# Kernel tuning notes

Hardware: AMD Instinct MI355X
Metric: run time of the kernel (lower is better)

The kernel has to match this reference:

```python
import jax, jax.numpy as jnp
import numpy as np

B, T = 8, 1024
D = 256          # n_embd
NH = 4           # n_head
MULT = 4         # mlp_internal_dim_multiplier
GRID = 32        # grid_size, T == GRID*GRID
NLAYER = 3
N = D * MULT // NH   # sparse head dim = 256
EPS = 1e-5


def _freqs_2d(h, w, dim, theta=10000.0):
    # matches get_freqs_2d_fixed: returns (h*w, dim//2) complex64
    dim_half = dim // 2
    freqs = 1.0 / theta ** (np.arange(0, dim_half, 2, dtype=np.float32) / dim_half)
    fx = np.outer(np.arange(w, dtype=np.float32), freqs)
    fy = np.outer(np.arange(h, dtype=np.float32), freqs)
    cx = np.exp(1j * fx).astype(np.complex64)          # (w, dim_half/2)
    cy = np.exp(1j * fy).astype(np.complex64)          # (h, dim_half/2)
    gx = np.broadcast_to(cx[None, :, :], (h, w, cx.shape[-1]))
    gy = np.broadcast_to(cy[:, None, :], (h, w, cy.shape[-1]))
    return np.concatenate([gx, gy], axis=-1).reshape(h * w, -1)

FREQS = jnp.asarray(_freqs_2d(GRID, GRID, N))  # (T, N//2) complex64


def _rope(x):
    # x: (B, nh, T, N) real -> complex pairs, rotate, back to real
    xc = x.reshape(*x.shape[:-1], -1, 2)
    xc = jax.lax.complex(xc[..., 0], xc[..., 1])       # (B, nh, T, N/2)
    xr = xc * FREQS[None, None, :, :]
    out = jnp.stack([jnp.real(xr), jnp.imag(xr)], axis=-1)
    return out.reshape(x.shape).astype(x.dtype)


def _ln(x):
    # LayerNorm over last dim, no affine (biased variance, like torch)
    m = jnp.mean(x, axis=-1, keepdims=True)
    v = jnp.var(x, axis=-1, keepdims=True)
    return (x - m) / jnp.sqrt(v + EPS)


def setup_inputs() -> dict:
    key = jax.random.key(0)
    ks = jax.random.split(key, 6)
    std = 0.02
    return {
        "inputs": jax.random.normal(ks[0], (B, T), dtype=jnp.float32),
        "in_w": jax.random.normal(ks[1], (D, 1), dtype=jnp.float32) * std,
        "in_b": jnp.zeros((D,), dtype=jnp.float32),
        "encoder": jax.random.normal(ks[2], (NH, D, N), dtype=jnp.float32) * std,
        "encoder_v": jax.random.normal(ks[3], (NH, D, N), dtype=jnp.float32) * std,
        "decoder": jax.random.normal(ks[4], (NH * N, D), dtype=jnp.float32) * std,
        "out_w": jax.random.normal(ks[5], (1, D), dtype=jnp.float32) * std,
        "out_b": jnp.zeros((1,), dtype=jnp.float32),
    }


def reference(inputs, in_w, in_b, encoder, encoder_v, decoder, out_w, out_b):
    # input projection: (B,T,1) @ (1,D) + b -> (B,T,D)
    x = inputs[..., None] * in_w[None, None, :, 0].swapaxes(-1, -1)  # placeholder
    x = inputs[..., None] @ in_w.T + in_b                            # (B,T,D)
    x = _ln(x)
    scale = 1.0 / jnp.sqrt(jnp.asarray(N, dtype=x.dtype))
    for _ in range(NLAYER):
        # encoder: (B,T,D) x (nh,D,N) -> (B,nh,T,N)
        x_sparse = jax.nn.relu(jnp.einsum('btd,hdn->bhtn', x, encoder))
        QR = _rope(x_sparse)
        KR = _rope(x_sparse)
        scores = jnp.einsum('bhtn,bhsn->bhts', QR, KR) * scale       # (B,nh,T,T)
        attn = jax.nn.softmax(scores, axis=-1)
        yKV = jnp.einsum('bhts,bsd->bhtd', attn, x)                  # V = x, broadcast over heads
        yKV = _ln(yKV)
        y_sparse = jax.nn.relu(jnp.einsum('bhtd,hdn->bhtn', yKV, encoder_v))
        xy_sparse = x_sparse * y_sparse                              # (B,nh,T,N)
        # (B,nh,T,N) -> (B,T,nh*N) @ (nh*N,D) -> (B,T,D)
        yMLP = xy_sparse.transpose(0, 2, 1, 3).reshape(B, T, NH * N) @ decoder
        x = _ln(x + _ln(yMLP))
    logits = x @ out_w.T + out_b                                     # (B,T,1)
    return logits
```

## Files before the change

kernel.cpp:

```cpp
#include <hip/hip_runtime.h>
#include <hip/hip_bf16.h>
#include <math.h>

#define B_ 8
#define T_ 1024
#define D_ 256
#define NH_ 4
#define N_ 256
#define EPS_ 1e-5f

typedef __attribute__((ext_vector_type(8))) short short8_t;
typedef __attribute__((ext_vector_type(4))) float floatx4;

__device__ inline unsigned short f2bf(float f) {
    unsigned u = __builtin_bit_cast(unsigned, f);
    u += 0x7FFFu + ((u >> 16) & 1u);
    return (unsigned short)(u >> 16);
}
__device__ inline float bf2f(unsigned short h) {
    return __builtin_bit_cast(float, (unsigned)h << 16);
}

__device__ inline void gload_lds16(const unsigned short* g, unsigned short* l) {
    __builtin_amdgcn_global_load_lds(
        (const __attribute__((address_space(1))) unsigned int*)g,
        (__attribute__((address_space(3))) unsigned int*)l, 16, 0, 0);
}

__device__ inline float2 block_stats_256(float v, float* red) {
    float s1 = v, s2 = v * v;
    #pragma unroll
    for (int o = 32; o > 0; o >>= 1) { s1 += __shfl_down(s1, o); s2 += __shfl_down(s2, o); }
    int wave = threadIdx.x >> 6, lane = threadIdx.x & 63;
    __syncthreads();
    if (lane == 0) { red[wave] = s1; red[4 + wave] = s2; }
    __syncthreads();
    float S1 = red[0] + red[1] + red[2] + red[3];
    float S2 = red[4] + red[5] + red[6] + red[7];
    float mean = S1 * (1.f / 256.f);
    float var  = S2 * (1.f / 256.f) - mean * mean;
    return make_float2(mean, var);
}

__global__ __launch_bounds__(256) void k_wT(
    const float* __restrict__ in, unsigned short* __restrict__ outh,
    unsigned short* __restrict__ outl, int R, int C)
{
    __shared__ float tile[64][65];
    int c0 = blockIdx.x * 64, r0 = blockIdx.y * 64, h = blockIdx.z;
    in += (size_t)h * R * C;
    for (int i = threadIdx.x; i < 4096; i += 256) {
        int r = i >> 6, c = i & 63;
        tile[r][c] = in[(size_t)(r0 + r) * C + c0 + c];
    }
    __syncthreads();
    for (int i = threadIdx.x; i < 4096; i += 256) {
        int c = i >> 6, r = i & 63;
        float v = tile[r][c];
        unsigned short hb = f2bf(v);
        size_t o = (size_t)(h * C + c0 + c) * R + r0 + r;
        outh[o] = hb;
        outl[o] = f2bf(v - bf2f(hb));
    }
}

__global__ __launch_bounds__(256) void k_input_ln(
    const float* __restrict__ inputs, const float* __restrict__ in_w,
    const float* __restrict__ in_b, float* __restrict__ x,
    unsigned short* __restrict__ xh, unsigned short* __restrict__ xl)
{
    __shared__ float red[8];
    int row = blockIdx.x;
    int d = threadIdx.x;
    float v = inputs[row] * in_w[d] + in_b[d];
    float2 mv = block_stats_256(v, red);
    float o = (v - mv.x) * rsqrtf(mv.y + EPS_);
    size_t idx = (size_t)row * D_ + d;
    x[idx] = o;
    unsigned short hb = f2bf(o);
    xh[idx] = hb;
    xl[idx] = f2bf(o - bf2f(hb));
}

#define PG 40
template<int MODE>
__global__ __launch_bounds__(256, 2) void k_gemm_mfma(
    const unsigned short* __restrict__ Ah, const unsigned short* __restrict__ Al,
    const unsigned short* __restrict__ Wh, const unsigned short* __restrict__ Wl,
    const unsigned short* __restrict__ xsh, const unsigned short* __restrict__ xsl,
    unsigned short* __restrict__ outh, unsigned short* __restrict__ outl,
    float* __restrict__ outf)
{
    constexpr int K = (MODE == 2) ? 1024 : 256;
    __shared__ unsigned short As_h[128 * PG], As_l[128 * PG];
    __shared__ unsigned short Ws_h[128 * PG], Ws_l[128 * PG];
    int tid = threadIdx.x;
    int w = tid >> 6, lane = tid & 63, quad = lane >> 4, l16 = lane & 15;
    int wm = w >> 1, wn = w & 1;
    int m0 = blockIdx.y * 128, n0x = blockIdx.x * 128;
    size_t a_row0, w_row0, out_row0;
    int col0;
    int koff = 0, kend = K;
    if (MODE == 1) {
        int bh = blockIdx.z;
        a_row0 = (size_t)bh * 1024 + m0;
        w_row0 = (size_t)((bh & 3) * 256 + n0x);
        out_row0 = (size_t)(bh >> 2) * 1024 + m0;
        col0 = (bh & 3) * 256 + n0x;
    } else {
        a_row0 = m0; w_row0 = n0x; out_row0 = m0; col0 = n0x;
        if (MODE == 2) { koff = blockIdx.z * 256; kend = koff + 256; }
    }
    floatx4 acc[4][4];
    #pragma unroll
    for (int mt = 0; mt < 4; mt++)
        #pragma unroll
        for (int nt = 0; nt < 4; nt++)
            acc[mt][nt] = (floatx4){0.f, 0.f, 0.f, 0.f};

    for (int k0 = koff; k0 < kend; k0 += 32) {
        #pragma unroll
        for (int it = 0; it < 2; it++) {
            int fl = tid + it * 256;
            int row = fl >> 2, ch = fl & 3;
            size_t ga = (a_row0 + row) * (size_t)K + k0 + ch * 8;
            size_t gw = (w_row0 + row) * (size_t)K + k0 + ch * 8;
            *(short8_t*)&As_h[row * PG + ch * 8] = *(const short8_t*)(Ah + ga);
            *(short8_t*)&As_l[row * PG + ch * 8] = *(const short8_t*)(Al + ga);
            *(short8_t*)&Ws_h[row * PG + ch * 8] = *(const short8_t*)(Wh + gw);
            *(short8_t*)&Ws_l[row * PG + ch * 8] = *(const short8_t*)(Wl + gw);
        }
        __syncthreads();
        short8_t afh[4], afl[4], bfh[4], bfl[4];
        #pragma unroll
        for (int mt = 0; mt < 4; mt++) {
            afh[mt] = *(const short8_t*)&As_h[(wm * 64 + mt * 16 + l16) * PG + quad * 8];
            afl[mt] = *(const short8_t*)&As_l[(wm * 64 + mt * 16 + l16) * PG + quad * 8];
        }
        #pragma unroll
        for (int nt = 0; nt < 4; nt++) {
            bfh[nt] = *(const short8_t*)&Ws_h[(wn * 64 + nt * 16 + l16) * PG + quad * 8];
            bfl[nt] = *(const short8_t*)&Ws_l[(wn * 64 + nt * 16 + l16) * PG + quad * 8];
        }
        #pragma unroll
        for (int mt = 0; mt < 4; mt++)
            #pragma unroll
            for (int nt = 0; nt < 4; nt++) {
                acc[mt][nt] = __builtin_amdgcn_mfma_f32_16x16x32_bf16(afh[mt], bfh[nt], acc[mt][nt], 0, 0, 0);
                acc[mt][nt] = __builtin_amdgcn_mfma_f32_16x16x32_bf16(afh[mt], bfl[nt], acc[mt][nt], 0, 0, 0);
                acc[mt][nt] = __builtin_amdgcn_mfma_f32_16x16x32_bf16(afl[mt], bfh[nt], acc[mt][nt], 0, 0, 0);
            }
        __syncthreads();
    }

    #pragma unroll
    for (int mt = 0; mt < 4; mt++) {
        #pragma unroll
        for (int r = 0; r < 4; r++) {
            size_t grow = out_row0 + wm * 64 + mt * 16 + quad * 4 + r;
            #pragma unroll
            for (int nt = 0; nt < 4; nt++) {
                int gcol = col0 + wn * 64 + nt * 16 + l16;
                float v = acc[mt][nt][r];
                if (MODE == 0) {
                    v = fmaxf(v, 0.f);
                    size_t o = grow * 1024 + gcol;
                    unsigned short hb = f2bf(v);
                    outh[o] = hb;
                    outl[o] = f2bf(v - bf2f(hb));
                } else if (MODE == 1) {
                    float y = fmaxf(v, 0.f);
                    size_t o = grow * 1024 + gcol;
                    float xv = bf2f(xsh[o]) + bf2f(xsl[o]);
                    float p = xv * y;
                    unsigned short hb = f2bf(p);
                    outh[o] = hb;
                    outl[o] = f2bf(p - bf2f(hb));
                } else {
                    outf[(size_t)blockIdx.z * 2097152 + grow * 256 + gcol] = v;
                }
            }
        }
    }
}

__global__ __launch_bounds__(256) void k_rope_bf16(
    const unsigned short* __restrict__ xsh, const unsigned short* __restrict__ xsl,
    unsigned short* __restrict__ qh, unsigned short* __restrict__ ql)
{
    int tid = blockIdx.x * 256 + threadIdx.x;
    int e0 = tid * 8;
    int n0 = e0 & 255;
    int t  = (e0 >> 8) & 1023;
    int bh = e0 >> 18;
    int h = bh & 3, b = bh >> 2;
    size_t src = (((size_t)(b * T_ + t) * NH_ + h) << 8) + n0;
    short8_t vh = *(const short8_t*)(xsh + src);
    short8_t vl = *(const short8_t*)(xsl + src);
    float v[8];
    #pragma unroll
    for (int i = 0; i < 8; i++)
        v[i] = bf2f((unsigned short)vh[i]) + bf2f((unsigned short)vl[i]);
    float cc[4], ss[4];
    int p0 = n0 >> 1;
    #pragma unroll
    for (int i = 0; i < 4; i++) {
        int p = p0 + i;
        int j = p & 63;
        int pos = (p < 64) ? (t & 31) : (t >> 5);
        float f = powf(10000.f, -(float)j * (1.f / 64.f));
        float ang = (float)pos * f;
        sincosf(ang, &ss[i], &cc[i]);
    }
    float r[8];
    r[0] = v[0] * cc[0] - v[1] * ss[0];
    r[1] = v[0] * ss[0] + v[1] * cc[0];
    r[2] = v[2] * cc[1] - v[3] * ss[1];
    r[3] = v[2] * ss[1] + v[3] * cc[1];
    r[4] = v[4] * cc[2] - v[5] * ss[2];
    r[5] = v[4] * ss[2] + v[5] * cc[2];
    r[6] = v[6] * cc[3] - v[7] * ss[3];
    r[7] = v[6] * ss[3] + v[7] * cc[3];
    short8_t oh, ol;
    #pragma unroll
    for (int i = 0; i < 8; i++) {
        unsigned short hbits = f2bf(r[i]);
        oh[i] = (short)hbits;
        ol[i] = (short)f2bf(r[i] - bf2f(hbits));
    }
    *(short8_t*)(qh + e0) = oh;
    *(short8_t*)(ql + e0) = ol;
}

__global__ __launch_bounds__(256) void k_xT(const float* __restrict__ x,
                                            unsigned short* __restrict__ Vfh,
                                            unsigned short* __restrict__ Vfl)
{
    __shared__ float tile[64][65];
    int t0 = blockIdx.x * 64, d0 = blockIdx.y * 64, b = blockIdx.z;
    const float* src = x + ((size_t)b * T_ + t0) * D_ + d0;
    for (int i = threadIdx.x; i < 1024; i += 256) {
        int r = i >> 4, c = i & 15;
        float4 v = *(const float4*)(src + (size_t)r * D_ + c * 4);
        tile[r][c * 4 + 0] = v.x;
        tile[r][c * 4 + 1] = v.y;
        tile[r][c * 4 + 2] = v.z;
        tile[r][c * 4 + 3] = v.w;
    }
    __syncthreads();
    for (int i = threadIdx.x; i < 1024; i += 256) {
        int d = i >> 4, c = i & 15;
        int tg = t0 + c * 4;
        int jj = tg >> 5, qd = (tg >> 3) & 3, i8 = tg & 7;
        int dg = d0 + d;
        int tn = dg >> 4, s16 = dg & 15;
        size_t o = (((size_t)b * 32 + jj) * 16 + tn) * 512 + (qd * 16 + s16) * 8 + i8;
        float v0 = tile[c * 4 + 0][d], v1 = tile[c * 4 + 1][d];
        float v2 = tile[c * 4 + 2][d], v3 = tile[c * 4 + 3][d];
        ushort4 oh, ol;
        oh.x = f2bf(v0); ol.x = f2bf(v0 - bf2f(oh.x));
        oh.y = f2bf(v1); ol.y = f2bf(v1 - bf2f(oh.y));
        oh.z = f2bf(v2); ol.z = f2bf(v2 - bf2f(oh.z));
        oh.w = f2bf(v3); ol.w = f2bf(v3 - bf2f(oh.w));
        *(ushort4*)(Vfh + o) = oh;
        *(ushort4*)(Vfl + o) = ol;
    }
}

#define PPW 36

__global__ __launch_bounds__(512, 1) void k_attn_mfma(
    const unsigned short* __restrict__ qr_h, const unsigned short* __restrict__ qr_l,
    const unsigned short* __restrict__ Vf_h, const unsigned short* __restrict__ Vf_l,
    unsigned short* __restrict__ ykvh, unsigned short* __restrict__ ykvl)
{
    __shared__ unsigned short K_h[2][16 * 512];
    __shared__ unsigned short K_l[2][16 * 512];
    __shared__ unsigned short V_h[2][16 * 512];
    __shared__ unsigned short V_l[2][16 * 512];
    __shared__ unsigned short P_h[8][16 * PPW];
    __shared__ unsigned short P_l[8][16 * PPW];

    int tid = threadIdx.x;
    int w = tid >> 6, lane = tid & 63, quad = lane >> 4, l16 = lane & 15;
    int gid = blockIdx.x;
    int bh = gid & 31, tile = gid >> 5, b = bh >> 2;
    int t0q = tile * 128;
    const unsigned short* qhb = qr_h + (size_t)bh * T_ * N_;
    const unsigned short* qlb = qr_l + (size_t)bh * T_ * N_;
    const unsigned short* vhb = Vf_h + (size_t)b * 32 * 16 * 512;
    const unsigned short* vlb = Vf_l + (size_t)b * 32 * 16 * 512;

    short8_t qfh[8], qfl[8];
    #pragma unroll
    for (int kc = 0; kc < 8; kc++) {
        size_t o = (size_t)(t0q + w * 16 + l16) * N_ + kc * 32 + quad * 8;
        qfh[kc] = *(const short8_t*)(qhb + o);
        qfl[kc] = *(const short8_t*)(qlb + o);
    }

    floatx4 O[16];
    #pragma unroll
    for (int tn = 0; tn < 16; tn++) O[tn] = (floatx4){0.f, 0.f, 0.f, 0.f};
    float lst[4] = {0.f, 0.f, 0.f, 0.f};
    const float scale = 0.0625f;

    #pragma unroll
    for (int s = 0; s < 2; s++) {
        int slot = w * 2 + s;
        int ct = slot >> 3, kc = slot & 7;
        size_t go = (size_t)(ct * 16 + l16) * N_ + kc * 32 + quad * 8;
        gload_lds16(qhb + go, &K_h[0][slot * 512]);
        gload_lds16(qlb + go, &K_l[0][slot * 512]);
        size_t vo = ((size_t)slot << 9) + lane * 8;
        gload_lds16(vhb + vo, &V_h[0][slot * 512]);
        gload_lds16(vlb + vo, &V_l[0][slot * 512]);
    }

    for (int j = 0; j < 32; j++) {
        int buf = j & 1;
        __syncthreads();
        if (j < 31) {
            #pragma unroll
            for (int s = 0; s < 2; s++) {
                int slot = w * 2 + s;
                int ct = slot >> 3, kc = slot & 7;
                size_t go = (size_t)((j + 1) * 32 + ct * 16 + l16) * N_ + kc * 32 + quad * 8;
                gload_lds16(qhb + go, &K_h[buf ^ 1][slot * 512]);
                gload_lds16(qlb + go, &K_l[buf ^ 1][slot * 512]);
                size_t vo = ((size_t)((j + 1) * 16 + slot) << 9) + lane * 8;
                gload_lds16(vhb + vo, &V_h[buf ^ 1][slot * 512]);
                gload_lds16(vlb + vo, &V_l[buf ^ 1][slot * 512]);
            }
        }

        floatx4 sc[2];
        #pragma unroll
        for (int ct = 0; ct < 2; ct++) {
            floatx4 a_hh = (floatx4){0.f, 0.f, 0.f, 0.f};
            floatx4 a_hl = (floatx4){0.f, 0.f, 0.f, 0.f};
            floatx4 a_lh = (floatx4){0.f, 0.f, 0.f, 0.f};
            #pragma unroll
            for (int kc = 0; kc < 8; kc++) {
                short8_t bkh = *(const short8_t*)&K_h[buf][(ct * 8 + kc) * 512 + lane * 8];
                short8_t bkl = *(const short8_t*)&K_l[buf][(ct * 8 + kc) * 512 + lane * 8];
                a_hh = __builtin_amdgcn_mfma_f32_16x16x32_bf16(qfh[kc], bkh, a_hh, 0, 0, 0);
                a_hl = __builtin_amdgcn_mfma_f32_16x16x32_bf16(qfh[kc], bkl, a_hl, 0, 0, 0);
                a_lh = __builtin_amdgcn_mfma_f32_16x16x32_bf16(qfl[kc], bkh, a_lh, 0, 0, 0);
            }
            sc[ct] = (a_hh + a_hl) + a_lh;
        }

        #pragma unroll
        for (int r = 0; r < 4; r++) {
            float p0 = __expf(sc[0][r] * scale - 8.f);
            float p1 = __expf(sc[1][r] * scale - 8.f);
            lst[r] += p0 + p1;
            unsigned short p0h = f2bf(p0), p1h = f2bf(p1);
            P_h[w][(quad * 4 + r) * PPW + l16]      = p0h;
            P_h[w][(quad * 4 + r) * PPW + 16 + l16] = p1h;
            P_l[w][(quad * 4 + r) * PPW + l16]      = f2bf(p0 - bf2f(p0h));
            P_l[w][(quad * 4 + r) * PPW + 16 + l16] = f2bf(p1 - bf2f(p1h));
        }

        short8_t pah = *(const short8_t*)&P_h[w][l16 * PPW + quad * 8];
        short8_t pal = *(const short8_t*)&P_l[w][l16 * PPW + quad * 8];

        #pragma unroll
        for (int tn = 0; tn < 16; tn++) {
            short8_t vbh = *(const short8_t*)&V_h[buf][tn * 512 + lane * 8];
            short8_t vbl = *(const short8_t*)&V_l[buf][tn * 512 + lane * 8];
            O[tn] = __builtin_amdgcn_mfma_f32_16x16x32_bf16(pah, vbh, O[tn], 0, 0, 0);
            O[tn] = __builtin_amdgcn_mfma_f32_16x16x32_bf16(pah, vbl, O[tn], 0, 0, 0);
            O[tn] = __builtin_amdgcn_mfma_f32_16x16x32_bf16(pal, vbh, O[tn], 0, 0, 0);
        }
    }

    size_t obase = ((size_t)bh * T_ + t0q + w * 16) * D_;
    #pragma unroll
    for (int r = 0; r < 4; r++) {
        float lsum = lst[r];
        #pragma unroll
        for (int o = 1; o < 16; o <<= 1) lsum += __shfl_xor(lsum, o);
        float li = 1.f / lsum;
        float s1 = 0.f, s2 = 0.f;
        #pragma unroll
        for (int tn = 0; tn < 16; tn++) { float v = O[tn][r]; s1 += v; s2 += v * v; }
        #pragma unroll
        for (int o = 1; o < 16; o <<= 1) { s1 += __shfl_xor(s1, o); s2 += __shfl_xor(s2, o); }
        float mean = s1 * li * (1.f / 256.f);
        float e2   = s2 * li * li * (1.f / 256.f);
        float var  = e2 - mean * mean;
        float rs = rsqrtf(var + EPS_);
        float a = li * rs, bb = mean * rs;
        int row = quad * 4 + r;
        #pragma unroll
        for (int tn = 0; tn < 16; tn++) {
            float v = O[tn][r] * a - bb;
            size_t o = obase + (size_t)row * D_ + tn * 16 + l16;
            unsigned short hb = f2bf(v);
            ykvh[o] = hb;
            ykvl[o] = f2bf(v - bf2f(hb));
        }
    }
}

__global__ __launch_bounds__(256) void k_resid_ln(float* __restrict__ x,
                                                  const float* __restrict__ ymlp,
                                                  unsigned short* __restrict__ xh,
                                                  unsigned short* __restrict__ xl)
{
    __shared__ float red[8];
    int row = blockIdx.x, d = threadIdx.x;
    size_t o = (size_t)row * D_ + d;
    float y = ymlp[o] + ymlp[o + 2097152] + ymlp[o + 2 * 2097152] + ymlp[o + 3 * 2097152];
    float2 mv1 = block_stats_256(y, red);
    float v = x[o] + (y - mv1.x) * rsqrtf(mv1.y + EPS_);
    float2 mv2 = block_stats_256(v, red);
    float out = (v - mv2.x) * rsqrtf(mv2.y + EPS_);
    x[o] = out;
    unsigned short hb = f2bf(out);
    xh[o] = hb;
    xl[o] = f2bf(out - bf2f(hb));
}

__global__ __launch_bounds__(256) void k_logits(
    const float* __restrict__ x, const float* __restrict__ out_w,
    const float* __restrict__ out_b, float* __restrict__ out)
{
    __shared__ float red[4];
    int row = blockIdx.x, d = threadIdx.x;
    float v = x[(size_t)row * D_ + d] * out_w[d];
    #pragma unroll
    for (int o = 32; o > 0; o >>= 1) v += __shfl_down(v, o);
    int wave = d >> 6, lane = d & 63;
    if (lane == 0) red[wave] = v;
    __syncthreads();
    if (d == 0) out[row] = red[0] + red[1] + red[2] + red[3] + out_b[0];
}

extern "C" void kernel_launch(void* const* d_in, const int* in_sizes, int n_in,
                              void* d_out, int out_size, void* d_ws, size_t ws_size,
                              hipStream_t stream)
{
    (void)in_sizes; (void)n_in; (void)out_size;
    if (ws_size < ((size_t)115 << 20)) return;

    const float* inputs    = (const float*)d_in[0];
    const float* in_w      = (const float*)d_in[1];
    const float* in_b      = (const float*)d_in[2];
    const float* encoder   = (const float*)d_in[3];
    const float* encoder_v = (const float*)d_in[4];
    const float* decoder   = (const float*)d_in[5];
    const float* out_w     = (const float*)d_in[6];
    const float* out_b     = (const float*)d_in[7];

    char* wsb = (char*)d_ws;
    float* x             = (float*)(wsb);
    unsigned short* x_h  = (unsigned short*)(wsb + ((size_t)8  << 20));
    unsigned short* x_l  = (unsigned short*)(wsb + ((size_t)12 << 20));
    unsigned short* Vf_h = x_h;
    unsigned short* Vf_l = x_l;
    unsigned short* xs_h = (unsigned short*)(wsb + ((size_t)16 << 20));
    unsigned short* xs_l = (unsigned short*)(wsb + ((size_t)32 << 20));
    float* ymlp          = (float*)(wsb + ((size_t)16 << 20));
    unsigned short* qr_h = (unsigned short*)(wsb + ((size_t)48 << 20));
    unsigned short* qr_l = (unsigned short*)(wsb + ((size_t)64 << 20));
    unsigned short* xy_h = qr_h;
    unsigned short* xy_l = qr_l;
    unsigned short* ykv_h = (unsigned short*)(wsb + ((size_t)80 << 20));
    unsigned short* ykv_l = (unsigned short*)(wsb + ((size_t)96 << 20));
    char* wbase = wsb + ((size_t)112 << 20);
    unsigned short* encT_h = (unsigned short*)(wbase);
    unsigned short* encT_l = (unsigned short*)(wbase + 0x80000);
    unsigned short* evT_h  = (unsigned short*)(wbase + 2 * 0x80000);
    unsigned short* evT_l  = (unsigned short*)(wbase + 3 * 0x80000);
    unsigned short* decT_h = (unsigned short*)(wbase + 4 * 0x80000);
    unsigned short* decT_l = (unsigned short*)(wbase + 5 * 0x80000);

    k_wT<<<dim3(4, 4, 4), 256, 0, stream>>>(encoder,   encT_h, encT_l, 256, 256);
    k_wT<<<dim3(4, 4, 4), 256, 0, stream>>>(encoder_v, evT_h,  evT_l,  256, 256);
    k_wT<<<dim3(4, 16, 1), 256, 0, stream>>>(decoder,  decT_h, decT_l, 1024, 256);

    k_input_ln<<<B_ * T_, 256, 0, stream>>>(inputs, in_w, in_b, x, x_h, x_l);
    for (int l = 0; l < 3; l++) {
        k_gemm_mfma<0><<<dim3(8, 64, 1), 256, 0, stream>>>(
            x_h, x_l, encT_h, encT_l, nullptr, nullptr, xs_h, xs_l, nullptr);
        k_rope_bf16<<<4096, 256, 0, stream>>>(xs_h, xs_l, qr_h, qr_l);
        k_xT<<<dim3(16, 4, 8), 256, 0, stream>>>(x, Vf_h, Vf_l);
        k_attn_mfma<<<256, 512, 0, stream>>>(qr_h, qr_l, Vf_h, Vf_l, ykv_h, ykv_l);
        k_gemm_mfma<1><<<dim3(2, 8, 32), 256, 0, stream>>>(
            ykv_h, ykv_l, evT_h, evT_l, xs_h, xs_l, xy_h, xy_l, nullptr);
        k_gemm_mfma<2><<<dim3(2, 64, 4), 256, 0, stream>>>(
            xy_h, xy_l, decT_h, decT_l, nullptr, nullptr, nullptr, nullptr, ymlp);
        k_resid_ln<<<B_ * T_, 256, 0, stream>>>(x, ymlp, x_h, x_l);
    }
    k_logits<<<B_ * T_, 256, 0, stream>>>(x, out_w, out_b, (float*)d_out);
}
```

Baseline: 765.7 us.

## Double-buffer GEMM tiles with direct global-to-LDS loads in MFMA kernel

Replaces the register-staged global-to-shared copies in the split-bf16 MFMA GEMM with global_load_lds direct loads into a fragment-ordered LDS layout. Tiles are double-buffered: the next K-slice is prefetched while MFMAs run on the current buffer, leaving one barrier per iteration. This aims to hide global load latency and cut VGPR traffic and LDS bank conflicts. LDS use doubles, which may lower occupancy, and correctness depends on the async load completing before the barrier.

```diff
diff --git a/kernel.cpp b/kernel.cpp
--- a/kernel.cpp
+++ b/kernel.cpp
@@ -82,7 +82,6 @@
     xl[idx] = f2bf(o - bf2f(hb));
 }
 
-#define PG 40
 template<int MODE>
 __global__ __launch_bounds__(256, 2) void k_gemm_mfma(
     const unsigned short* __restrict__ Ah, const unsigned short* __restrict__ Al,
@@ -92,8 +91,8 @@
     float* __restrict__ outf)
 {
     constexpr int K = (MODE == 2) ? 1024 : 256;
-    __shared__ unsigned short As_h[128 * PG], As_l[128 * PG];
-    __shared__ unsigned short Ws_h[128 * PG], Ws_l[128 * PG];
+    __shared__ unsigned short As_h[2][8 * 512], As_l[2][8 * 512];
+    __shared__ unsigned short Ws_h[2][8 * 512], Ws_l[2][8 * 512];
     int tid = threadIdx.x;
     int w = tid >> 6, lane = tid & 63, quad = lane >> 4, l16 = lane & 15;
     int wm = w >> 1, wn = w & 1;
@@ -111,6 +110,18 @@
         a_row0 = m0; w_row0 = n0x; out_row0 = m0; col0 = n0x;
         if (MODE == 2) { koff = blockIdx.z * 256; kend = koff + 256; }
     }
+
+    #pragma unroll
+    for (int s = 0; s < 2; s++) {
+        int slot = w * 2 + s;
+        size_t ga = (a_row0 + slot * 16 + l16) * (size_t)K + koff + quad * 8;
+        size_t gw = (w_row0 + slot * 16 + l16) * (size_t)K + koff + quad * 8;
+        gload_lds16(Ah + ga, &As_h[0][slot * 512]);
+        gload_lds16(Al + ga, &As_l[0][slot * 512]);
+        gload_lds16(Wh + gw, &Ws_h[0][slot * 512]);
+        gload_lds16(Wl + gw, &Ws_l[0][slot * 512]);
+    }
+
     floatx4 acc[4][4];
     #pragma unroll
     for (int mt = 0; mt < 4; mt++)
@@ -118,29 +129,33 @@
         for (int nt = 0; nt < 4; nt++)
             acc[mt][nt] = (floatx4){0.f, 0.f, 0.f, 0.f};
 
-    for (int k0 = koff; k0 < kend; k0 += 32) {
-        #pragma unroll
-        for (int it = 0; it < 2; it++) {
-            int fl = tid + it * 256;
-            int row = fl >> 2, ch = fl & 3;
-            size_t ga = (a_row0 + row) * (size_t)K + k0 + ch * 8;
-            size_t gw = (w_row0 + row) * (size_t)K + k0 + ch * 8;
-            *(short8_t*)&As_h[row * PG + ch * 8] = *(const short8_t*)(Ah + ga);
-            *(short8_t*)&As_l[row * PG + ch * 8] = *(const short8_t*)(Al + ga);
-            *(short8_t*)&Ws_h[row * PG + ch * 8] = *(const short8_t*)(Wh + gw);
-            *(short8_t*)&Ws_l[row * PG + ch * 8] = *(const short8_t*)(Wl + gw);
-        }
+    const int nIter = (kend - koff) >> 5;
+    for (int it = 0; it < nIter; it++) {
+        int buf = it & 1;
         __syncthreads();
+        if (it + 1 < nIter) {
+            int k1 = koff + (it + 1) * 32;
+            #pragma unroll
+            for (int s = 0; s < 2; s++) {
+                int slot = w * 2 + s;
+                size_t ga = (a_row0 + slot * 16 + l16) * (size_t)K + k1 + quad * 8;
+                size_t gw = (w_row0 + slot * 16 + l16) * (size_t)K + k1 + quad * 8;
+                gload_lds16(Ah + ga, &As_h[buf ^ 1][slot * 512]);
+                gload_lds16(Al + ga, &As_l[buf ^ 1][slot * 512]);
+                gload_lds16(Wh + gw, &Ws_h[buf ^ 1][slot * 512]);
+                gload_lds16(Wl + gw, &Ws_l[buf ^ 1][slot * 512]);
+            }
+        }
         short8_t afh[4], afl[4], bfh[4], bfl[4];
         #pragma unroll
         for (int mt = 0; mt < 4; mt++) {
-            afh[mt] = *(const short8_t*)&As_h[(wm * 64 + mt * 16 + l16) * PG + quad * 8];
-            afl[mt] = *(const short8_t*)&As_l[(wm * 64 + mt * 16 + l16) * PG + quad * 8];
+            afh[mt] = *(const short8_t*)&As_h[buf][(wm * 4 + mt) * 512 + lane * 8];
+            afl[mt] = *(const short8_t*)&As_l[buf][(wm * 4 + mt) * 512 + lane * 8];
         }
         #pragma unroll
         for (int nt = 0; nt < 4; nt++) {
-            bfh[nt] = *(const short8_t*)&Ws_h[(wn * 64 + nt * 16 + l16) * PG + quad * 8];
-            bfl[nt] = *(const short8_t*)&Ws_l[(wn * 64 + nt * 16 + l16) * PG + quad * 8];
+            bfh[nt] = *(const short8_t*)&Ws_h[buf][(wn * 4 + nt) * 512 + lane * 8];
+            bfl[nt] = *(const short8_t*)&Ws_l[buf][(wn * 4 + nt) * 512 + lane * 8];
         }
         #pragma unroll
         for (int mt = 0; mt < 4; mt++)
@@ -150,7 +165,6 @@
                 acc[mt][nt] = __builtin_amdgcn_mfma_f32_16x16x32_bf16(afh[mt], bfl[nt], acc[mt][nt], 0, 0, 0);
                 acc[mt][nt] = __builtin_amdgcn_mfma_f32_16x16x32_bf16(afl[mt], bfh[nt], acc[mt][nt], 0, 0, 0);
             }
-        __syncthreads();
     }
 
     #pragma unroll
```

After: 836.2 us. 9.2% more time.
